# Kernel tuning notes

Hardware: AMD Instinct MI355X
Metric: run time of the kernel (lower is better)

Reference implementation:

```python
import jax, jax.numpy as jnp
import numpy as np

H = 16          # num_heads
EPS = 1e-6      # RMSNorm eps


def _rms_norm(t, w):
    # t: [..., head_dim], w: [head_dim]
    var = jnp.mean(jnp.square(t), axis=-1, keepdims=True)
    return t * jax.lax.rsqrt(var + EPS) * w


def setup_inputs() -> dict:
    key = jax.random.key(0)
    ks = jax.random.split(key, 8)
    B, N, M, C = 2, 2048, 256, 1024
    s = 0.02
    return {
        "x": jax.random.normal(ks[0], (B, N, C), jnp.float32),
        "y": jax.random.normal(ks[1], (B, M, C), jnp.float32),
        "qkv_w": jax.random.normal(ks[2], (3 * C, C), jnp.float32) * s,
        "qkv_b": jax.random.normal(ks[3], (3 * C,), jnp.float32) * s,
        "kv_w": jax.random.normal(ks[4], (2 * C, C), jnp.float32) * s,
        "kv_b": jax.random.normal(ks[5], (2 * C,), jnp.float32) * s,
        "qn_w": jnp.ones((C // H,), jnp.float32),
        "kn_w": jnp.ones((C // H,), jnp.float32),
        "proj_w": jax.random.normal(ks[6], (C, C), jnp.float32) * s,
        "proj_b": jax.random.normal(ks[7], (C,), jnp.float32) * s,
    }


def reference(x, y, qkv_w, qkv_b, kv_w, kv_b, qn_w, kn_w, proj_w, proj_b):
    B, N, C = x.shape
    M = y.shape[1]
    hd = C // H
    scale = hd ** -0.5

    # fused QKV projection for image tokens -> [B, H, N, hd] each
    qkv = (jnp.einsum('bnc,oc->bno', x, qkv_w) + qkv_b).reshape(B, N, 3, H, hd)
    qkv = jnp.transpose(qkv, (2, 0, 3, 1, 4))
    q, kx, vx = qkv[0], qkv[1], qkv[2]

    # qk-norm (RMSNorm over head_dim)
    q = _rms_norm(q, qn_w)
    kx = _rms_norm(kx, kn_w)

    # KV projection for text tokens -> [B, H, M, hd] each
    kvy = (jnp.einsum('bmc,oc->bmo', y, kv_w) + kv_b).reshape(B, M, 2, H, hd)
    kvy = jnp.transpose(kvy, (2, 0, 3, 1, 4))
    ky, vy = kvy[0], kvy[1]
    ky = _rms_norm(ky, kn_w)

    # concat image+text KV along the sequence axis
    k = jnp.concatenate([kx, ky], axis=2)  # [B, H, N+M, hd]
    v = jnp.concatenate([vx, vy], axis=2)

    # scaled dot-product attention
    logits = jnp.einsum('bhnd,bhsd->bhns', q, k) * scale  # [B, H, N, N+M]
    attn = jax.nn.softmax(logits, axis=-1)
    out = jnp.einsum('bhns,bhsd->bhnd', attn, v)          # [B, H, N, hd]

    out = jnp.transpose(out, (0, 2, 1, 3)).reshape(B, N, C)
    return jnp.einsum('bnc,oc->bno', out, proj_w) + proj_b
```

## Files before the change

kernel.cpp:

```cpp
#include <hip/hip_runtime.h>

#define BATCH 2
#define NTOK 2048
#define MTOK 256
#define CDIM 1024
#define NHEAD 16
#define HD 64
#define SEQ (NTOK + MTOK)
#define TOK_X (BATCH * NTOK)
#define TOK_Y (BATCH * MTOK)
#define BHN (BATCH * NHEAD)
#define NKT (SEQ / 64)
#define QKV_BLOCKS 1536
#define KV_BLOCKS 128

typedef __attribute__((ext_vector_type(8))) short bf16x8;
typedef __attribute__((ext_vector_type(4))) short bf16x4;
typedef __attribute__((ext_vector_type(4))) float f32x4;
typedef __attribute__((ext_vector_type(2))) unsigned int u32x2;
typedef __attribute__((ext_vector_type(4))) unsigned int u32x4;
#if __has_builtin(__builtin_amdgcn_cvt_pk_bf16_f32)
typedef __attribute__((ext_vector_type(2))) __bf16 bf16x2_t;
#endif

__device__ __forceinline__ float b2f(ushort u) {
    unsigned v = ((unsigned)u) << 16;
    return __builtin_bit_cast(float, v);
}
__device__ __forceinline__ ushort f2b(float f) {
    unsigned u = __builtin_bit_cast(unsigned, f);
    u += 0x7fffu + ((u >> 16) & 1u);
    return (ushort)(u >> 16);
}
__device__ __forceinline__ unsigned pack2bf(float a, float b) {
#if __has_builtin(__builtin_amdgcn_cvt_pk_bf16_f32)
    bf16x2_t h = __builtin_amdgcn_cvt_pk_bf16_f32(a, b);
    return __builtin_bit_cast(unsigned, h);
#else
    return ((unsigned)f2b(b) << 16) | (unsigned)f2b(a);
#endif
}

__device__ __forceinline__ void async_load16(const ushort* g, ushort* l) {
    __builtin_amdgcn_global_load_lds(
        (const __attribute__((address_space(1))) unsigned*)(const void*)g,
        (__attribute__((address_space(3))) unsigned*)(void*)l, 16, 0, 0);
}

__global__ __launch_bounds__(256) void cast_all(
    const float* __restrict__ s0, ushort* __restrict__ t0, int b0,
    const float* __restrict__ s1, ushort* __restrict__ t1, int b1,
    const float* __restrict__ s2, ushort* __restrict__ t2, int b2,
    const float* __restrict__ s3, ushort* __restrict__ t3, int b3,
    const float* __restrict__ s4, ushort* __restrict__ t4) {
    int blk = blockIdx.x;
    const float* s; ushort* t;
    if (blk < b0)      { s = s0; t = t0; }
    else if (blk < b1) { s = s1; t = t1; blk -= b0; }
    else if (blk < b2) { s = s2; t = t2; blk -= b1; }
    else if (blk < b3) { s = s3; t = t3; blk -= b2; }
    else               { s = s4; t = t4; blk -= b3; }
    int i = (blk * 256 + threadIdx.x) * 8;
    float4 a = *(const float4*)(s + i);
    float4 b = *(const float4*)(s + i + 4);
    ushort tmp[8] = {f2b(a.x), f2b(a.y), f2b(a.z), f2b(a.w),
                     f2b(b.x), f2b(b.y), f2b(b.z), f2b(b.w)};
    *(uint4*)(t + i) = *(const uint4*)tmp;
}

__global__ __launch_bounds__(256) void gemm_qkvkv(const ushort* __restrict__ Aq,
                                                  const ushort* __restrict__ Wq,
                                                  const float* __restrict__ bq,
                                                  const ushort* __restrict__ Ak,
                                                  const ushort* __restrict__ Wk,
                                                  const float* __restrict__ bk,
                                                  ushort* __restrict__ d_q,
                                                  ushort* __restrict__ d_k,
                                                  ushort* __restrict__ d_vt,
                                                  const float* __restrict__ qn_w,
                                                  const float* __restrict__ kn_w) {
    __shared__ ushort As[128][64];
    __shared__ ushort Bs[64][64];
    int tid = threadIdx.x;
    int lane = tid & 63;
    int w = tid >> 6;
    int wm = w * 32;
    int l15 = lane & 15;
    int quad = lane >> 4;
    int sw = l15 & 7;

    int blk = blockIdx.x;
    int mode, bx, by;
    const ushort *A, *Bt;
    const float* bias;
    if (blk < QKV_BLOCKS) {
        mode = 1;
        int xcd = blk & 7;
        int loc = blk >> 3;
        by = xcd * 4 + (loc & 3);
        bx = loc >> 2;
        A = Aq; Bt = Wq; bias = bq;
    } else {
        mode = 2;
        int loc = blk - QKV_BLOCKS;
        bx = loc & 31;
        by = loc >> 5;
        A = Ak; Bt = Wk; bias = bk;
    }
    int bm = by * 128;
    int bn = bx * 64;

    f32x4 acc[2][4];
#pragma unroll
    for (int i = 0; i < 2; i++)
#pragma unroll
        for (int j = 0; j < 4; j++) acc[i][j] = (f32x4)0.0f;

    int lrow = lane >> 3;
    int lcol = ((lane & 7) ^ lrow) * 8;

    for (int k0 = 0; k0 < CDIM; k0 += 64) {
        __syncthreads();
#pragma unroll
        for (int p = 0; p < 4; p++) {
            int rb = w * 32 + p * 8;
            async_load16(&A[(size_t)(bm + rb + lrow) * CDIM + k0 + lcol], &As[rb][0]);
        }
#pragma unroll
        for (int p = 0; p < 2; p++) {
            int rb = w * 16 + p * 8;
            async_load16(&Bt[(size_t)(bn + rb + lrow) * CDIM + k0 + lcol], &Bs[rb][0]);
        }
        __syncthreads();
#pragma unroll
        for (int kk = 0; kk < 64; kk += 32) {
            bf16x8 af[2], bfr[4];
            int g = (kk >> 3) + quad;
            int csw = (g ^ sw) * 8;
#pragma unroll
            for (int i = 0; i < 2; i++)
                af[i] = *(const bf16x8*)&As[wm + i * 16 + l15][csw];
#pragma unroll
            for (int j = 0; j < 4; j++)
                bfr[j] = *(const bf16x8*)&Bs[j * 16 + l15][csw];
#pragma unroll
            for (int i = 0; i < 2; i++)
#pragma unroll
                for (int j = 0; j < 4; j++)
                    acc[i][j] = __builtin_amdgcn_mfma_f32_16x16x32_bf16(af[i], bfr[j], acc[i][j], 0, 0, 0);
        }
    }

    float bv[4];
#pragma unroll
    for (int j = 0; j < 4; j++) bv[j] = bias[bn + j * 16 + l15];
#pragma unroll
    for (int i = 0; i < 2; i++)
#pragma unroll
        for (int j = 0; j < 4; j++)
#pragma unroll
            for (int r = 0; r < 4; r++) acc[i][j][r] += bv[j];

    int region = bn >> 10;
    int h = (bn >> 6) & (NHEAD - 1);
    bool is_q = (mode == 1) && (region == 0);
    bool is_k = (mode == 1) ? (region == 1) : (region == 0);
    if (is_q || is_k) {
        const float* wv = is_q ? qn_w : kn_w;
        float wj[4];
#pragma unroll
        for (int j = 0; j < 4; j++) wj[j] = wv[j * 16 + l15];
        float qs = is_q ? (0.125f * 1.44269504088896f) : 1.0f;
#pragma unroll
        for (int i = 0; i < 2; i++)
#pragma unroll
            for (int r = 0; r < 4; r++) {
                float s = acc[i][0][r] * acc[i][0][r] + acc[i][1][r] * acc[i][1][r]
                        + acc[i][2][r] * acc[i][2][r] + acc[i][3][r] * acc[i][3][r];
                s += __shfl_xor(s, 1);
                s += __shfl_xor(s, 2);
                s += __shfl_xor(s, 4);
                s += __shfl_xor(s, 8);
                float rs = rsqrtf(s * (1.0f / 64.0f) + 1e-6f) * qs;
#pragma unroll
                for (int j = 0; j < 4; j++) acc[i][j][r] *= rs * wj[j];
            }
    }
    size_t l15seq = (size_t)l15 * SEQ;
#pragma unroll
    for (int i = 0; i < 2; i++) {
#pragma unroll
        for (int r = 0; r < 4; r++) {
            int t = bm + wm + i * 16 + quad * 4 + r;
            int b, s;
            if (mode == 1) { b = t >> 11; s = t & (NTOK - 1); }
            else           { b = t >> 8;  s = NTOK + (t & (MTOK - 1)); }
            size_t bh = (size_t)(b * NHEAD + h);
            if (is_q) {
                size_t base = (bh * NTOK + s) * 64;
#pragma unroll
                for (int j = 0; j < 4; j++)
                    d_q[base + j * 16 + l15] = f2b(acc[i][j][r]);
            } else if (is_k) {
                size_t base = (bh * SEQ + s) * 64;
#pragma unroll
                for (int j = 0; j < 4; j++)
                    d_k[base + j * 16 + l15] = f2b(acc[i][j][r]);
            } else {
                int within = s & 31;
                int pos = ((s >> 5) << 5) + ((within & 15) << 1) + (within >> 4);
                size_t base = bh * 64 * SEQ + l15seq + pos;
#pragma unroll
                for (int j = 0; j < 4; j++)
                    d_vt[base + (size_t)(j * 16) * SEQ] = f2b(acc[i][j][r]);
            }
        }
    }
}

__global__ __launch_bounds__(256) void gemm_proj(const ushort* __restrict__ A,
                                                 const ushort* __restrict__ Bt,
                                                 const float* __restrict__ bias,
                                                 float* __restrict__ Cf) {
    __shared__ ushort As[128][64];
    __shared__ ushort Bs[64][64];
    int tid = threadIdx.x;
    int lane = tid & 63;
    int w = tid >> 6;
    int wm = w * 32;
    int l15 = lane & 15;
    int quad = lane >> 4;
    int sw = l15 & 7;
    int xcd = blockIdx.x & 7;
    int loc = blockIdx.x >> 3;
    int by = xcd * 4 + (loc & 3);
    int bx = loc >> 2;
    int bm = by * 128;
    int bn = bx * 64;

    f32x4 acc[2][4];
#pragma unroll
    for (int i = 0; i < 2; i++)
#pragma unroll
        for (int j = 0; j < 4; j++) acc[i][j] = (f32x4)0.0f;

    int lrow = lane >> 3;
    int lcol = ((lane & 7) ^ lrow) * 8;

    for (int k0 = 0; k0 < CDIM; k0 += 64) {
        __syncthreads();
#pragma unroll
        for (int p = 0; p < 4; p++) {
            int rb = w * 32 + p * 8;
            async_load16(&A[(size_t)(bm + rb + lrow) * CDIM + k0 + lcol], &As[rb][0]);
        }
#pragma unroll
        for (int p = 0; p < 2; p++) {
            int rb = w * 16 + p * 8;
            async_load16(&Bt[(size_t)(bn + rb + lrow) * CDIM + k0 + lcol], &Bs[rb][0]);
        }
        __syncthreads();
#pragma unroll
        for (int kk = 0; kk < 64; kk += 32) {
            bf16x8 af[2], bfr[4];
            int g = (kk >> 3) + quad;
            int csw = (g ^ sw) * 8;
#pragma unroll
            for (int i = 0; i < 2; i++)
                af[i] = *(const bf16x8*)&As[wm + i * 16 + l15][csw];
#pragma unroll
            for (int j = 0; j < 4; j++)
                bfr[j] = *(const bf16x8*)&Bs[j * 16 + l15][csw];
#pragma unroll
            for (int i = 0; i < 2; i++)
#pragma unroll
                for (int j = 0; j < 4; j++)
                    acc[i][j] = __builtin_amdgcn_mfma_f32_16x16x32_bf16(af[i], bfr[j], acc[i][j], 0, 0, 0);
        }
    }
#pragma unroll
    for (int i = 0; i < 2; i++) {
        int row0 = bm + wm + i * 16 + quad * 4;
#pragma unroll
        for (int j = 0; j < 4; j++) {
            int col = bn + j * 16 + l15;
            float bvv = bias[col];
#pragma unroll
            for (int r = 0; r < 4; r++)
                Cf[(size_t)(row0 + r) * CDIM + col] = acc[i][j][r] + bvv;
        }
    }
}

__global__ __launch_bounds__(256) void attn_fwd(const ushort* __restrict__ qh,
                                                const ushort* __restrict__ kc,
                                                const ushort* __restrict__ vt,
                                                ushort* __restrict__ out) {
    __shared__ ushort Ks[2][64][72];
    __shared__ ushort Vs[2][64][68];
    int tid = threadIdx.x;
    int lane = tid & 63;
    int w = tid >> 6;
    int l15 = lane & 15;
    int quad = lane >> 4;
    int bh = blockIdx.y;
    int q0 = blockIdx.x * 128 + w * 32;

    const ushort* qpA = qh + ((size_t)bh * NTOK + q0 + l15) * 64 + quad * 8;
    const ushort* qpB = qpA + 16 * 64;
    bf16x8 qA0 = *(const bf16x8*)qpA;
    bf16x8 qA1 = *(const bf16x8*)(qpA + 32);
    bf16x8 qB0 = *(const bf16x8*)qpB;
    bf16x8 qB1 = *(const bf16x8*)(qpB + 32);

    float lA = 0.0f, lB = 0.0f;
    f32x4 OA[4], OB[4];
#pragma unroll
    for (int jd = 0; jd < 4; jd++) { OA[jd] = (f32x4)0.0f; OB[jd] = (f32x4)0.0f; }

    int sr = tid >> 3, sc = (tid & 7) * 8;
    const ushort* kp0 = kc + (size_t)bh * SEQ * 64 + (size_t)sr * 64 + sc;
    const ushort* kp1 = kp0 + (size_t)32 * 64;
    const ushort* vp0 = vt + (size_t)bh * 64 * SEQ + (size_t)sr * SEQ + sc;
    const ushort* vp1 = vp0 + (size_t)32 * SEQ;

    uint4 rka = *(const uint4*)kp0;
    uint4 rkb = *(const uint4*)kp1;
    uint4 rva = *(const uint4*)vp0;
    uint4 rvb = *(const uint4*)vp1;

    for (int t = 0; t < NKT; t++) {
        int p = t & 1;
        *(uint4*)&Ks[p][sr][sc] = rka;
        *(uint4*)&Ks[p][sr + 32][sc] = rkb;
        *(uint4*)&Vs[p][sr][sc] = rva;
        *(uint4*)&Vs[p][sr + 32][sc] = rvb;
        __syncthreads();
        if (t + 1 < NKT) {
            kp0 += 64 * 64; kp1 += 64 * 64; vp0 += 64; vp1 += 64;
            rka = *(const uint4*)kp0;
            rkb = *(const uint4*)kp1;
            rva = *(const uint4*)vp0;
            rvb = *(const uint4*)vp1;
        }

        f32x4 SA[4], SB[4];
#pragma unroll
        for (int j = 0; j < 4; j++) { SA[j] = (f32x4)0.0f; SB[j] = (f32x4)0.0f; }
        __builtin_amdgcn_s_setprio(1);
#pragma unroll
        for (int j = 0; j < 4; j++) {
            bf16x8 kf = *(const bf16x8*)&Ks[p][j * 16 + l15][quad * 8];
            SA[j] = __builtin_amdgcn_mfma_f32_16x16x32_bf16(kf, qA0, SA[j], 0, 0, 0);
            SB[j] = __builtin_amdgcn_mfma_f32_16x16x32_bf16(kf, qB0, SB[j], 0, 0, 0);
        }
#pragma unroll
        for (int j = 0; j < 4; j++) {
            bf16x8 kf = *(const bf16x8*)&Ks[p][j * 16 + l15][32 + quad * 8];
            SA[j] = __builtin_amdgcn_mfma_f32_16x16x32_bf16(kf, qA1, SA[j], 0, 0, 0);
            SB[j] = __builtin_amdgcn_mfma_f32_16x16x32_bf16(kf, qB1, SB[j], 0, 0, 0);
        }
        __builtin_amdgcn_s_setprio(0);

#pragma unroll
        for (int pb2 = 0; pb2 < 2; pb2++) {
            int j0 = 2 * pb2, j1 = j0 + 1;
            u32x4 wa, wb;
#pragma unroll
            for (int r = 0; r < 4; r++) {
                float a0 = __builtin_amdgcn_exp2f(SA[j0][r]);
                float a1 = __builtin_amdgcn_exp2f(SA[j1][r]);
                lA += a0 + a1;
                wa[r] = pack2bf(a0, a1);
                float b0 = __builtin_amdgcn_exp2f(SB[j0][r]);
                float b1 = __builtin_amdgcn_exp2f(SB[j1][r]);
                lB += b0 + b1;
                wb[r] = pack2bf(b0, b1);
            }
            bf16x8 pA = __builtin_bit_cast(bf16x8, wa);
            bf16x8 pB = __builtin_bit_cast(bf16x8, wb);
            __builtin_amdgcn_s_setprio(1);
#pragma unroll
            for (int jd = 0; jd < 4; jd++) {
                bf16x8 vf = *(const bf16x8*)&Vs[p][jd * 16 + l15][pb2 * 32 + quad * 8];
                OA[jd] = __builtin_amdgcn_mfma_f32_16x16x32_bf16(vf, pA, OA[jd], 0, 0, 0);
                OB[jd] = __builtin_amdgcn_mfma_f32_16x16x32_bf16(vf, pB, OB[jd], 0, 0, 0);
            }
            __builtin_amdgcn_s_setprio(0);
        }
    }
    lA += __shfl_xor(lA, 16);
    lA += __shfl_xor(lA, 32);
    lB += __shfl_xor(lB, 16);
    lB += __shfl_xor(lB, 32);
    float invA = 1.0f / lA;
    float invB = 1.0f / lB;
    int b = bh >> 4, h = bh & 15;
    int tokA = (b << 11) + q0 + l15;
    ushort* obaseA = out + ((size_t)tokA * NHEAD + h) * 64;
    ushort* obaseB = obaseA + (size_t)16 * NHEAD * 64;
#pragma unroll
    for (int jd = 0; jd < 4; jd++) {
        u32x2 pk;
        pk.x = pack2bf(OA[jd][0] * invA, OA[jd][1] * invA);
        pk.y = pack2bf(OA[jd][2] * invA, OA[jd][3] * invA);
        *(u32x2*)&obaseA[jd * 16 + quad * 4] = pk;
        pk.x = pack2bf(OB[jd][0] * invB, OB[jd][1] * invB);
        pk.y = pack2bf(OB[jd][2] * invB, OB[jd][3] * invB);
        *(u32x2*)&obaseB[jd * 16 + quad * 4] = pk;
    }
}

extern "C" void kernel_launch(void* const* d_in, const int* in_sizes, int n_in,
                              void* d_out, int out_size, void* d_ws, size_t ws_size,
                              hipStream_t stream) {
    const float* x      = (const float*)d_in[0];
    const float* y      = (const float*)d_in[1];
    const float* qkv_w  = (const float*)d_in[2];
    const float* qkv_b  = (const float*)d_in[3];
    const float* kv_w   = (const float*)d_in[4];
    const float* kv_b   = (const float*)d_in[5];
    const float* qn_w   = (const float*)d_in[6];
    const float* kn_w   = (const float*)d_in[7];
    const float* proj_w = (const float*)d_in[8];
    const float* proj_b = (const float*)d_in[9];
    float* outp = (float*)d_out;

    char* ws = (char*)d_ws;
    ushort* x_bf    = (ushort*)ws; ws += (size_t)TOK_X * CDIM * 2;
    ushort* y_bf    = (ushort*)ws; ws += (size_t)TOK_Y * CDIM * 2;
    ushort* qkvw_bf = (ushort*)ws; ws += (size_t)3 * CDIM * CDIM * 2;
    ushort* kvw_bf  = (ushort*)ws; ws += (size_t)2 * CDIM * CDIM * 2;
    ushort* projw_bf= (ushort*)ws; ws += (size_t)CDIM * CDIM * 2;
    ushort* qh      = (ushort*)ws; ws += (size_t)BHN * NTOK * 64 * 2;
    ushort* kc      = (ushort*)ws; ws += (size_t)BHN * SEQ * 64 * 2;
    ushort* vt      = (ushort*)ws; ws += (size_t)BHN * SEQ * 64 * 2;
    ushort* ao      = (ushort*)ws; ws += (size_t)TOK_X * CDIM * 2;

    int c0 = TOK_X * CDIM / 2048;
    int c1 = c0 + TOK_Y * CDIM / 2048;
    int c2 = c1 + 3 * CDIM * CDIM / 2048;
    int c3 = c2 + 2 * CDIM * CDIM / 2048;
    int c4 = c3 + CDIM * CDIM / 2048;
    cast_all<<<c4, 256, 0, stream>>>(x, x_bf, c0, y, y_bf, c1, qkv_w, qkvw_bf, c2,
                                     kv_w, kvw_bf, c3, proj_w, projw_bf);

    gemm_qkvkv<<<QKV_BLOCKS + KV_BLOCKS, 256, 0, stream>>>(
        x_bf, qkvw_bf, qkv_b, y_bf, kvw_bf, kv_b, qh, kc, vt, qn_w, kn_w);

    attn_fwd<<<dim3(NTOK / 128, BHN), 256, 0, stream>>>(qh, kc, vt, ao);

    gemm_proj<<<512, 256, 0, stream>>>(ao, projw_bf, proj_b, outp);
}
```

Measured before the change: 219.6 us.

## Software-pipeline attention: overlap QK of next tile with PV of previous tile

Restructures the attention inner loop so each iteration issues the QK MFMAs for tile i+1 together with the PV MFMAs for tile i, then runs the exp/pack for the new scores. V gets a triple buffer in shared memory so the previous tile's V stays valid while the next is staged. The aim is to hide the exp/softmax latency behind matrix-core work instead of serializing QK, softmax and PV. The cost is more shared memory and more live registers (packed P for two sub-blocks), which may reduce occupancy.

```diff
diff --git a/kernel.cpp b/kernel.cpp
--- a/kernel.cpp
+++ b/kernel.cpp
@@ -297,7 +297,7 @@
                                                 const ushort* __restrict__ vt,
                                                 ushort* __restrict__ out) {
     __shared__ ushort Ks[2][64][72];
-    __shared__ ushort Vs[2][64][68];
+    __shared__ ushort Vs[3][64][68];
     int tid = threadIdx.x;
     int lane = tid & 63;
     int w = tid >> 6;
@@ -329,39 +329,47 @@
     uint4 rva = *(const uint4*)vp0;
     uint4 rvb = *(const uint4*)vp1;
 
-    for (int t = 0; t < NKT; t++) {
-        int p = t & 1;
-        *(uint4*)&Ks[p][sr][sc] = rka;
-        *(uint4*)&Ks[p][sr + 32][sc] = rkb;
-        *(uint4*)&Vs[p][sr][sc] = rva;
-        *(uint4*)&Vs[p][sr + 32][sc] = rvb;
-        __syncthreads();
-        if (t + 1 < NKT) {
-            kp0 += 64 * 64; kp1 += 64 * 64; vp0 += 64; vp1 += 64;
-            rka = *(const uint4*)kp0;
-            rkb = *(const uint4*)kp1;
-            rva = *(const uint4*)vp0;
-            rvb = *(const uint4*)vp1;
-        }
-
-        f32x4 SA[4], SB[4];
-#pragma unroll
-        for (int j = 0; j < 4; j++) { SA[j] = (f32x4)0.0f; SB[j] = (f32x4)0.0f; }
-        __builtin_amdgcn_s_setprio(1);
+    auto stage = [&](int kb, int vb) {
+        *(uint4*)&Ks[kb][sr][sc] = rka;
+        *(uint4*)&Ks[kb][sr + 32][sc] = rkb;
+        *(uint4*)&Vs[vb][sr][sc] = rva;
+        *(uint4*)&Vs[vb][sr + 32][sc] = rvb;
+    };
+    auto advance_load = [&]() {
+        kp0 += 64 * 64; kp1 += 64 * 64; vp0 += 64; vp1 += 64;
+        rka = *(const uint4*)kp0;
+        rkb = *(const uint4*)kp1;
+        rva = *(const uint4*)vp0;
+        rvb = *(const uint4*)vp1;
+    };
+    auto qk_tile = [&](int kb, f32x4* SA, f32x4* SB) {
 #pragma unroll
         for (int j = 0; j < 4; j++) {
-            bf16x8 kf = *(const bf16x8*)&Ks[p][j * 16 + l15][quad * 8];
+            bf16x8 kf = *(const bf16x8*)&Ks[kb][j * 16 + l15][quad * 8];
             SA[j] = __builtin_amdgcn_mfma_f32_16x16x32_bf16(kf, qA0, SA[j], 0, 0, 0);
             SB[j] = __builtin_amdgcn_mfma_f32_16x16x32_bf16(kf, qB0, SB[j], 0, 0, 0);
         }
 #pragma unroll
         for (int j = 0; j < 4; j++) {
-            bf16x8 kf = *(const bf16x8*)&Ks[p][j * 16 + l15][32 + quad * 8];
+            bf16x8 kf = *(const bf16x8*)&Ks[kb][j * 16 + l15][32 + quad * 8];
             SA[j] = __builtin_amdgcn_mfma_f32_16x16x32_bf16(kf, qA1, SA[j], 0, 0, 0);
             SB[j] = __builtin_amdgcn_mfma_f32_16x16x32_bf16(kf, qB1, SB[j], 0, 0, 0);
         }
-        __builtin_amdgcn_s_setprio(0);
-
+    };
+
+    bf16x8 pA[2], pB[2];
+
+    auto pv_tile = [&](int vb) {
+#pragma unroll
+        for (int pb2 = 0; pb2 < 2; pb2++)
+#pragma unroll
+            for (int jd = 0; jd < 4; jd++) {
+                bf16x8 vf = *(const bf16x8*)&Vs[vb][jd * 16 + l15][pb2 * 32 + quad * 8];
+                OA[jd] = __builtin_amdgcn_mfma_f32_16x16x32_bf16(vf, pA[pb2], OA[jd], 0, 0, 0);
+                OB[jd] = __builtin_amdgcn_mfma_f32_16x16x32_bf16(vf, pB[pb2], OB[jd], 0, 0, 0);
+            }
+    };
+    auto softmax_pack = [&](const f32x4* SA, const f32x4* SB) {
 #pragma unroll
         for (int pb2 = 0; pb2 < 2; pb2++) {
             int j0 = 2 * pb2, j1 = j0 + 1;
@@ -377,18 +385,46 @@
                 lB += b0 + b1;
                 wb[r] = pack2bf(b0, b1);
             }
-            bf16x8 pA = __builtin_bit_cast(bf16x8, wa);
-            bf16x8 pB = __builtin_bit_cast(bf16x8, wb);
-            __builtin_amdgcn_s_setprio(1);
-#pragma unroll
-            for (int jd = 0; jd < 4; jd++) {
-                bf16x8 vf = *(const bf16x8*)&Vs[p][jd * 16 + l15][pb2 * 32 + quad * 8];
-                OA[jd] = __builtin_amdgcn_mfma_f32_16x16x32_bf16(vf, pA, OA[jd], 0, 0, 0);
-                OB[jd] = __builtin_amdgcn_mfma_f32_16x16x32_bf16(vf, pB, OB[jd], 0, 0, 0);
-            }
-            __builtin_amdgcn_s_setprio(0);
-        }
-    }
+            pA[pb2] = __builtin_bit_cast(bf16x8, wa);
+            pB[pb2] = __builtin_bit_cast(bf16x8, wb);
+        }
+    };
+
+    stage(0, 0);
+    advance_load();
+    __syncthreads();
+    {
+        f32x4 SA[4], SB[4];
+#pragma unroll
+        for (int j = 0; j < 4; j++) { SA[j] = (f32x4)0.0f; SB[j] = (f32x4)0.0f; }
+        __builtin_amdgcn_s_setprio(1);
+        qk_tile(0, SA, SB);
+        __builtin_amdgcn_s_setprio(0);
+        softmax_pack(SA, SB);
+    }
+
+    int vr = 0;
+    for (int i = 0; i < NKT - 1; i++) {
+        int kb = (i + 1) & 1;
+        int vw = vr + 1; if (vw == 3) vw = 0;
+        stage(kb, vw);
+        if (i < NKT - 2) advance_load();
+        __syncthreads();
+
+        f32x4 SA[4], SB[4];
+#pragma unroll
+        for (int j = 0; j < 4; j++) { SA[j] = (f32x4)0.0f; SB[j] = (f32x4)0.0f; }
+        __builtin_amdgcn_s_setprio(1);
+        qk_tile(kb, SA, SB);
+        pv_tile(vr);
+        __builtin_amdgcn_s_setprio(0);
+        softmax_pack(SA, SB);
+        vr = vw;
+    }
+    __builtin_amdgcn_s_setprio(1);
+    pv_tile(vr);
+    __builtin_amdgcn_s_setprio(0);
+
     lA += __shfl_xor(lA, 16);
     lA += __shfl_xor(lA, 32);
     lB += __shfl_xor(lB, 16);
```

Result: no change. 220.4 us (+0.3%).
